# Optimization experiments

Measured on AMD Instinct MI355X. Metric: run time of the kernel, lower is better.

The kernel has to match this reference:

```python
import jax, jax.numpy as jnp
import numpy as np
import math

B, S, D_MODEL, NHEAD, DFF = 4, 1024, 1024, 16, 4096
D_K = D_MODEL // NHEAD
EPS = 1e-5
FACTOR = 5  # ProbAttention factor


def setup_inputs() -> dict:
    key = jax.random.key(0)
    ks = jax.random.split(key, 16)
    def w(k, shape):
        return 0.02 * jax.random.normal(k, shape, jnp.float32)
    inp = {
        "tgt": jax.random.normal(ks[0], (B, S, D_MODEL), jnp.float32),
        "memory": jax.random.normal(ks[1], (B, S, D_MODEL), jnp.float32),
    }
    i = 2
    for n in ["sa_wq", "sa_wk", "sa_wv", "sa_wo", "ca_wq", "ca_wk", "ca_wv", "ca_wo"]:
        inp[n] = w(ks[i], (D_MODEL, D_MODEL)); i += 1
        inp[n.replace("_w", "_b")] = jnp.zeros((D_MODEL,), jnp.float32)
    inp["w1"] = w(ks[i], (D_MODEL, DFF)); i += 1
    inp["b1"] = jnp.zeros((DFF,), jnp.float32)
    inp["w2"] = w(ks[i], (DFF, D_MODEL)); i += 1
    inp["b2"] = jnp.zeros((D_MODEL,), jnp.float32)
    for j in (1, 2, 3):
        inp[f"bn{j}_g"] = jnp.ones((D_MODEL,), jnp.float32)
        inp[f"bn{j}_b"] = jnp.zeros((D_MODEL,), jnp.float32)
    return inp


def prob_attention(q, k, v, rng):
    # Informer ProbSparse attention, mask_flag=False. q,k,v: [B,H,L,D]
    Bq, H, Lq, D = q.shape
    Lk = k.shape[2]
    sample_k = min(FACTOR * int(math.ceil(math.log(Lk))), Lk)
    n_top = min(FACTOR * int(math.ceil(math.log(Lq))), Lq)
    # sampled key indices per query position (shared across B,H, as in Informer)
    idx = jax.random.randint(rng, (Lq, sample_k), 0, Lk)
    k_samp = k[:, :, idx, :]                                 # [B,H,Lq,sample_k,D]
    qk_samp = jnp.einsum("bhld,bhlsd->bhls", q, k_samp)
    M = qk_samp.max(-1) - qk_samp.sum(-1) / Lk               # sparsity measure [B,H,Lq]
    top_idx = jax.lax.top_k(M, n_top)[1]                     # [B,H,n_top]
    q_red = jnp.take_along_axis(q, top_idx[..., None], axis=2)  # [B,H,n_top,D]
    scores = jnp.einsum("bhud,bhkd->bhuk", q_red, k) * (1.0 / math.sqrt(D))
    attn = jax.nn.softmax(scores, axis=-1)                   # [B,H,n_top,Lk]
    # initial context: mean of V for all queries, then overwrite the top queries
    ctx = jnp.broadcast_to(v.mean(axis=2, keepdims=True), (Bq, H, Lq, D))
    upd = jnp.einsum("bhuk,bhkd->bhud", attn, v)
    b_ix = jnp.arange(Bq)[:, None, None]
    h_ix = jnp.arange(H)[None, :, None]
    return ctx.at[b_ix, h_ix, top_idx].set(upd)


def mha(xq, xk, xv, wq, bq, wk, bk, wv, bv, wo, bo, rng):
    Bq, L, E = xq.shape
    def split(x, wt, bt):
        return (x @ wt + bt).reshape(Bq, L, NHEAD, D_K).transpose(0, 2, 1, 3)
    q, k, v = split(xq, wq, bq), split(xk, wk, bk), split(xv, wv, bv)
    o = prob_attention(q, k, v, rng)
    return o.transpose(0, 2, 1, 3).reshape(Bq, L, E) @ wo + bo


def bn(x, g, b):
    # BatchNorm1d over channel dim E, stats over (B, S) (training-mode, biased var)
    mu = x.mean(axis=(0, 1))
    var = x.var(axis=(0, 1))
    return (x - mu) * jax.lax.rsqrt(var + EPS) * g + b


def reference(tgt, memory, sa_wq, sa_bq, sa_wk, sa_bk, sa_wv, sa_bv, sa_wo, sa_bo,
              ca_wq, ca_bq, ca_wk, ca_bk, ca_wv, ca_bv, ca_wo, ca_bo,
              w1, b1, w2, b2, bn1_g, bn1_b, bn2_g, bn2_b, bn3_g, bn3_b):
    k1, k2 = jax.random.split(jax.random.key(42))
    t2 = mha(tgt, tgt, tgt, sa_wq, sa_bq, sa_wk, sa_bk, sa_wv, sa_bv, sa_wo, sa_bo, k1)
    x = bn(tgt + t2, bn1_g, bn1_b)
    t2 = mha(x, memory, memory, ca_wq, ca_bq, ca_wk, ca_bk, ca_wv, ca_bv, ca_wo, ca_bo, k2)
    x = bn(x + t2, bn2_g, bn2_b)
    t2 = jax.nn.gelu(x @ w1 + b1, approximate=False) @ w2 + b2
    return bn(x + t2, bn3_g, bn3_b)
```

## Files before the change

### kernel.cpp

```cpp
#include <hip/hip_runtime.h>
#include <cstdint>

#define BQ 4
#define SEQ 1024
#define EMB 1024
#define NH 16
#define DKH 64
#define DFF 4096
#define MROWS 4096
#define NSAMP 35
#define QKV_LD 3072

typedef int   i32x4 __attribute__((ext_vector_type(4)));
typedef float f32x4 __attribute__((ext_vector_type(4)));
typedef short s16x8 __attribute__((ext_vector_type(8)));
typedef __bf16 b16x8 __attribute__((ext_vector_type(8)));

__device__ __forceinline__ unsigned short bf16b(float f) {
  unsigned u = __builtin_bit_cast(unsigned, f);
  return (unsigned short)((u + 0x7FFFu + ((u >> 16) & 1u)) >> 16);
}

template <typename T> struct other_vec { using type = b16x8; };
template <> struct other_vec<b16x8>    { using type = s16x8; };

template <typename T>
__device__ __forceinline__ auto mfma_try(T a, T b, f32x4 c, int)
    -> decltype(__builtin_amdgcn_mfma_f32_16x16x32_bf16(a, b, c, 0, 0, 0)) {
  return __builtin_amdgcn_mfma_f32_16x16x32_bf16(a, b, c, 0, 0, 0);
}
template <typename T>
__device__ __forceinline__ f32x4 mfma_try(T a, T b, f32x4 c, long) {
  using U = typename other_vec<T>::type;
  U a2 = __builtin_bit_cast(U, a);
  U b2 = __builtin_bit_cast(U, b);
  return __builtin_amdgcn_mfma_f32_16x16x32_bf16(a2, b2, c, 0, 0, 0);
}
__device__ __forceinline__ f32x4 mfma_bf16(i32x4 a, i32x4 b, f32x4 c) {
  s16x8 as = __builtin_bit_cast(s16x8, a);
  s16x8 bs = __builtin_bit_cast(s16x8, b);
  return mfma_try(as, bs, c, 0);
}

typedef const __attribute__((address_space(1))) void GV;
typedef __attribute__((address_space(3))) void LV;
__device__ __forceinline__ void gload_lds16(const void* g, void* l) {
  __builtin_amdgcn_global_load_lds((GV*)(uintptr_t)g,
                                   (LV*)(unsigned)(uintptr_t)l, 16, 0, 0);
}

__device__ __forceinline__ void tf2x32(unsigned k0, unsigned k1, unsigned x0, unsigned x1,
                                       unsigned& o0, unsigned& o1) {
  unsigned ks2 = k0 ^ k1 ^ 0x1BD11BDAu;
  x0 += k0; x1 += k1;
#define TFR(r) { x0 += x1; x1 = (x1 << r) | (x1 >> (32 - r)); x1 ^= x0; }
  TFR(13) TFR(15) TFR(26) TFR(6)   x0 += k1;  x1 += ks2 + 1u;
  TFR(17) TFR(29) TFR(16) TFR(24)  x0 += ks2; x1 += k0 + 2u;
  TFR(13) TFR(15) TFR(26) TFR(6)   x0 += k0;  x1 += k1 + 3u;
  TFR(17) TFR(29) TFR(16) TFR(24)  x0 += k1;  x1 += ks2 + 4u;
  TFR(13) TFR(15) TFR(26) TFR(6)   x0 += ks2; x1 += k0 + 5u;
#undef TFR
  o0 = x0; o1 = x1;
}

__global__ void idx_kernel(int* __restrict__ out) {
  int t = blockIdx.x * 256 + threadIdx.x;
  if (t >= 2 * SEQ * NSAMP) return;
  int sel = t >= SEQ * NSAMP;
  int i = sel ? t - SEQ * NSAMP : t;
  unsigned s0, s1, d0, d1;
  tf2x32(0u, 42u, 0u, 0u, s0, s1);
  tf2x32(0u, 42u, 0u, 1u, d0, d1);
  unsigned key0 = sel ? d0 : s0, key1 = sel ? d1 : s1;
  unsigned o0, o1;
  tf2x32(key0, key1, 0u, (unsigned)i, o0, o1);
  out[t] = (int)((o0 ^ o1) & 1023u);
}

__global__ void f2b_kernel(const float* __restrict__ in, unsigned short* __restrict__ out, int n4) {
  int i = blockIdx.x * 256 + threadIdx.x;
  if (i >= n4) return;
  float4 v = ((const float4*)in)[i];
  uint2 p;
  p.x = (unsigned)bf16b(v.x) | ((unsigned)bf16b(v.y) << 16);
  p.y = (unsigned)bf16b(v.z) | ((unsigned)bf16b(v.w) << 16);
  ((uint2*)out)[i] = p;
}

__global__ void transpose_kernel(const float* __restrict__ W, unsigned short* __restrict__ WT,
                                 int K, int N) {
  __shared__ float tile[32][33];
  int n0 = blockIdx.x * 32, k0 = blockIdx.y * 32;
  int tx = threadIdx.x, ty = threadIdx.y;
#pragma unroll
  for (int r = 0; r < 4; ++r)
    tile[ty * 4 + r][tx] = W[(size_t)(k0 + ty * 4 + r) * N + n0 + tx];
  __syncthreads();
#pragma unroll
  for (int r = 0; r < 4; ++r) {
    int n = n0 + ty * 4 + r, k = k0 + tx;
    WT[(size_t)n * K + k] = bf16b(tile[tx][ty * 4 + r]);
  }
}

__global__ void biascat_kernel(const float* q, const float* k, const float* v,
                               const float* ck, const float* cv,
                               float* qkvB, float* kvB) {
  int t = blockIdx.x * 256 + threadIdx.x;
  if (t < 1024) {
    qkvB[t] = q[t]; qkvB[1024 + t] = k[t]; qkvB[2048 + t] = v[t];
    kvB[t] = ck[t]; kvB[1024 + t] = cv[t];
  }
}

template <int EPI>
__global__ __launch_bounds__(256) void gemm_kernel(
    const unsigned short* __restrict__ A, int lda,
    const unsigned short* __restrict__ BT, int ldb,
    float* __restrict__ C, int ldc,
    unsigned short* __restrict__ Cb, int ldcb,
    const float* __restrict__ bias, int K) {
  __shared__ alignas(16) unsigned short As[128 * 32];
  __shared__ alignas(16) unsigned short Bs[128 * 32];
  const int tid = threadIdx.x;
  const int bm = blockIdx.y << 7, bn = blockIdx.x << 7;
  const int wave = tid >> 6, lane = tid & 63;
  const int wm = (wave & 1) << 6, wn = (wave >> 1) << 6;
  const int lr = lane & 15, lg = lane >> 4;

  f32x4 acc[4][4];
#pragma unroll
  for (int i = 0; i < 4; ++i)
#pragma unroll
    for (int j = 0; j < 4; ++j) acc[i][j] = f32x4{0.f, 0.f, 0.f, 0.f};

  const int trow = tid >> 2, tcol = (tid & 3) << 3;
  const unsigned short* Ag = A + (size_t)(bm + trow) * lda + tcol;
  const unsigned short* Bg = BT + (size_t)(bn + trow) * ldb + tcol;
  unsigned short* Al = &As[tid * 8];
  unsigned short* Bl = &Bs[tid * 8];

  for (int kt = 0; kt < K; kt += 32) {
    __syncthreads();
    gload_lds16(Ag + kt, Al);
    gload_lds16(Ag + (size_t)64 * lda + kt, Al + 2048);
    gload_lds16(Bg + kt, Bl);
    gload_lds16(Bg + (size_t)64 * ldb + kt, Bl + 2048);
    __syncthreads();
    i32x4 af[4], bf[4];
#pragma unroll
    for (int i = 0; i < 4; ++i)
      af[i] = *(const i32x4*)&As[(wm + i * 16 + lr) * 32 + lg * 8];
#pragma unroll
    for (int j = 0; j < 4; ++j)
      bf[j] = *(const i32x4*)&Bs[(wn + j * 16 + lr) * 32 + lg * 8];
#pragma unroll
    for (int i = 0; i < 4; ++i)
#pragma unroll
      for (int j = 0; j < 4; ++j)
        acc[i][j] = mfma_bf16(af[i], bf[j], acc[i][j]);
  }
#pragma unroll
  for (int i = 0; i < 4; ++i)
#pragma unroll
    for (int j = 0; j < 4; ++j)
#pragma unroll
      for (int r = 0; r < 4; ++r) {
        int row = bm + wm + i * 16 + lg * 4 + r;
        int col = bn + wn + j * 16 + lr;
        float v = acc[i][j][r] + bias[col];
        if constexpr (EPI == 0) {
          C[(size_t)row * ldc + col] = v;
        } else {
          float gl = 0.5f * v * (1.f + erff(v * 0.70710678118654752f));
          Cb[(size_t)row * ldcb + col] = bf16b(gl);
        }
      }
}

__global__ __launch_bounds__(256) void m2_kernel(
    const float* __restrict__ QKV, const int* __restrict__ idx,
    float* __restrict__ Mout, int qcol, int kcol) {
  const int bh = blockIdx.y, qc = blockIdx.x;
  const int b = bh >> 4, h = bh & 15;
  const int tid = threadIdx.x, wv = tid >> 6, lane = tid & 63;
  const float* Qb = QKV + (size_t)b * SEQ * QKV_LD + qcol + h * 64;
  const float* Kb = QKV + (size_t)b * SEQ * QKV_LD + kcol + h * 64;
  const bool act = lane < NSAMP;
  for (int j = 0; j < 32; ++j) {
    int l = qc * 128 + wv * 32 + j;
    float dot = 0.f;
    if (act) {
      int sidx = idx[l * NSAMP + lane];
      const float* Kr = Kb + (size_t)sidx * QKV_LD;
      const float* Qr = Qb + (size_t)l * QKV_LD;
#pragma unroll
      for (int d4 = 0; d4 < 16; ++d4) {
        float4 k4 = *(const float4*)(Kr + d4 * 4);
        float4 q4 = *(const float4*)(Qr + d4 * 4);
        dot = fmaf(k4.x, q4.x, dot);
        dot = fmaf(k4.y, q4.y, dot);
        dot = fmaf(k4.z, q4.z, dot);
        dot = fmaf(k4.w, q4.w, dot);
      }
    }
    float mval = act ? dot : -__builtin_inff();
    float sval = act ? dot : 0.f;
#pragma unroll
    for (int m = 1; m < 64; m <<= 1) {
      mval = fmaxf(mval, __shfl_xor(mval, m, 64));
      sval += __shfl_xor(sval, m, 64);
    }
    if (lane == 0) Mout[bh * 1024 + l] = mval - sval * (1.f / 1024.f);
  }
}

__device__ __forceinline__ void amax2(float& v, int& id, float v2, int id2) {
  if (v2 > v || (v2 == v && id2 < id)) { v = v2; id = id2; }
}
__global__ __launch_bounds__(64) void topk2_kernel(
    const float* __restrict__ Mbuf, int* __restrict__ topOut) {
  const int bh = blockIdx.x, t = threadIdx.x;
  float v[16]; int li[16];
#pragma unroll
  for (int r = 0; r < 16; ++r) { int l = t + (r << 6); v[r] = Mbuf[bh * 1024 + l]; li[r] = l; }
  for (int it = 0; it < NSAMP; ++it) {
    float bv = v[0]; int bi = li[0];
#pragma unroll
    for (int r = 1; r < 16; ++r) amax2(bv, bi, v[r], li[r]);
#pragma unroll
    for (int m = 1; m < 64; m <<= 1) {
      float ov = __shfl_xor(bv, m, 64); int oi = __shfl_xor(bi, m, 64);
      amax2(bv, bi, ov, oi);
    }
    if (t == 0) topOut[bh * NSAMP + it] = bi;
#pragma unroll
    for (int r = 0; r < 16; ++r) if (li[r] == bi) v[r] = -__builtin_inff();
  }
}

__global__ void vmean_kernel(const float* __restrict__ QKV, float* __restrict__ vmean, int vcol) {
  const int g = blockIdx.x, bh = g >> 3, ch = g & 7;
  const int b = bh >> 4, h = bh & 15, d = threadIdx.x;
  const float* Vb = QKV + (size_t)b * SEQ * QKV_LD + vcol + h * 64 + d;
  float s = 0.f;
  for (int l = ch * 128; l < ch * 128 + 128; ++l) s += Vb[(size_t)l * QKV_LD];
  atomicAdd(&vmean[bh * 64 + d], s);
}

__global__ void fillO_kernel(const float* __restrict__ vmean, unsigned short* __restrict__ Ob) {
  int i = blockIdx.x * 256 + threadIdx.x;
  int e = i & 1023, b = i >> 20;
  int h = e >> 6, d = e & 63;
  Ob[i] = bf16b(vmean[((b << 4) + h) * 64 + d] * (1.f / 1024.f));
}

__global__ __launch_bounds__(256) void attn_part_kernel(
    const float* __restrict__ QKV, const int* __restrict__ topIdx,
    float* __restrict__ Opart, int qcol, int kcol, int vcol) {
  __shared__ int til[NSAMP];
  __shared__ alignas(16) float qs[NSAMP * 64];
  __shared__ alignas(16) float ps[NSAMP * 260];
  const int c = blockIdx.x, bh = blockIdx.y;
  const int b = bh >> 4, h = bh & 15;
  const int tid = threadIdx.x, wv = tid >> 6, lane = tid & 63;
  if (tid < NSAMP) til[tid] = topIdx[bh * NSAMP + tid];
  __syncthreads();
  for (int e = tid; e < NSAMP * 64; e += 256) {
    int i = e >> 6, d = e & 63;
    qs[e] = QKV[((size_t)b * SEQ + til[i]) * QKV_LD + qcol + h * 64 + d];
  }
  __syncthreads();
  {
    const float* Kr = QKV + ((size_t)b * SEQ + c * 256 + tid) * QKV_LD + kcol + h * 64;
    float acc[NSAMP];
#pragma unroll
    for (int i = 0; i < NSAMP; ++i) acc[i] = 0.f;
    for (int c16 = 0; c16 < 16; ++c16) {
      float4 k4 = *(const float4*)(Kr + c16 * 4);
#pragma unroll
      for (int i = 0; i < NSAMP; ++i) {
        float4 q4 = *(const float4*)&qs[i * 64 + c16 * 4];
        acc[i] = fmaf(k4.x, q4.x, acc[i]);
        acc[i] = fmaf(k4.y, q4.y, acc[i]);
        acc[i] = fmaf(k4.z, q4.z, acc[i]);
        acc[i] = fmaf(k4.w, q4.w, acc[i]);
      }
    }
#pragma unroll
    for (int i = 0; i < NSAMP; ++i) ps[i * 260 + tid] = expf(acc[i] * 0.125f);
  }
  __syncthreads();
  float o[NSAMP], sacc[NSAMP];
#pragma unroll
  for (int i = 0; i < NSAMP; ++i) { o[i] = 0.f; sacc[i] = 0.f; }
  {
    const float* Vb = QKV + ((size_t)b * SEQ + c * 256) * QKV_LD + vcol + h * 64 + lane;
    for (int j = 0; j < 64; ++j) {
      int kkl = wv * 64 + j;
      float vv = Vb[(size_t)kkl * QKV_LD];
#pragma unroll
      for (int i = 0; i < NSAMP; ++i) {
        float p = ps[i * 260 + kkl];
        o[i] = fmaf(p, vv, o[i]);
        sacc[i] += p;
      }
    }
  }
  __syncthreads();
  float* red = ps;
#pragma unroll
  for (int i = 0; i < NSAMP; ++i) {
    red[(wv * NSAMP + i) * 65 + lane] = o[i];
    if (lane == 0) red[(wv * NSAMP + i) * 65 + 64] = sacc[i];
  }
  __syncthreads();
  for (int e = tid; e < NSAMP * 65; e += 256) {
    int i = e / 65, d = e - i * 65;
    float s = red[(0 * NSAMP + i) * 65 + d] + red[(1 * NSAMP + i) * 65 + d] +
              red[(2 * NSAMP + i) * 65 + d] + red[(3 * NSAMP + i) * 65 + d];
    Opart[((size_t)(bh * NSAMP + i) * 4 + c) * 65 + d] = s;
  }
}

__global__ __launch_bounds__(256) void attn_final_kernel(
    const float* __restrict__ Opart, const int* __restrict__ topIdx,
    unsigned short* __restrict__ Ob) {
  int e = blockIdx.x * 256 + threadIdx.x;
  int d = e & 63, r = e >> 6;
  int bh = r / NSAMP, i = r - bh * NSAMP;
  const float* base = Opart + (size_t)r * 4 * 65;
  float s = base[d] + base[65 + d] + base[130 + d] + base[195 + d];
  float den = base[64] + base[129] + base[194] + base[259];
  int b = bh >> 4, h = bh & 15;
  int til = topIdx[r];
  Ob[((size_t)b * SEQ + til) * EMB + h * 64 + d] = bf16b(s / den);
}

__global__ __launch_bounds__(256) void bnstats_kernel(
    const float* __restrict__ a, const float* __restrict__ bb, float* __restrict__ sums) {
  const int t = threadIdx.x, r0 = blockIdx.x << 5;
  float s1[4] = {0, 0, 0, 0}, s2[4] = {0, 0, 0, 0};
  for (int r = r0; r < r0 + 32; ++r) {
    const float* ar = a + (size_t)r * EMB;
    const float* br = bb + (size_t)r * EMB;
#pragma unroll
    for (int q = 0; q < 4; ++q) {
      float x = ar[t + (q << 8)] + br[t + (q << 8)];
      s1[q] += x; s2[q] = fmaf(x, x, s2[q]);
    }
  }
#pragma unroll
  for (int q = 0; q < 4; ++q) {
    atomicAdd(&sums[t + (q << 8)], s1[q]);
    atomicAdd(&sums[EMB + t + (q << 8)], s2[q]);
  }
}
__global__ void bnapply_kernel(
    const float* __restrict__ a, const float* __restrict__ bres,
    const float* __restrict__ sums, const float* __restrict__ g,
    const float* __restrict__ bet, float* __restrict__ outF, unsigned short* __restrict__ outB) {
  int i = blockIdx.x * 256 + threadIdx.x;
  int c = i & (EMB - 1);
  float mu = sums[c] * (1.f / 4096.f);
  float var = sums[EMB + c] * (1.f / 4096.f) - mu * mu;
  float x = a[i] + bres[i];
  float y = (x - mu) * rsqrtf(var + 1e-5f) * g[c] + bet[c];
  outF[i] = y;
  if (outB) outB[i] = bf16b(y);
}

extern "C" void kernel_launch(void* const* d_in, const int* in_sizes, int n_in,
                              void* d_out, int out_size, void* d_ws, size_t ws_size,
                              hipStream_t stream) {
  const float* tgt  = (const float*)d_in[0];
  const float* memi = (const float*)d_in[1];
  const float* sa_wq = (const float*)d_in[2];  const float* sa_bq = (const float*)d_in[3];
  const float* sa_wk = (const float*)d_in[4];  const float* sa_bk = (const float*)d_in[5];
  const float* sa_wv = (const float*)d_in[6];  const float* sa_bv = (const float*)d_in[7];
  const float* sa_wo = (const float*)d_in[8];  const float* sa_bo = (const float*)d_in[9];
  const float* ca_wq = (const float*)d_in[10]; const float* ca_bq = (const float*)d_in[11];
  const float* ca_wk = (const float*)d_in[12]; const float* ca_bk = (const float*)d_in[13];
  const float* ca_wv = (const float*)d_in[14]; const float* ca_bv = (const float*)d_in[15];
  const float* ca_wo = (const float*)d_in[16]; const float* ca_bo = (const float*)d_in[17];
  const float* w1 = (const float*)d_in[18];    const float* b1 = (const float*)d_in[19];
  const float* w2 = (const float*)d_in[20];    const float* b2 = (const float*)d_in[21];
  const float* bn1g = (const float*)d_in[22];  const float* bn1b = (const float*)d_in[23];
  const float* bn2g = (const float*)d_in[24];  const float* bn2b = (const float*)d_in[25];
  const float* bn3g = (const float*)d_in[26];  const float* bn3b = (const float*)d_in[27];

  char* wsb = (char*)d_ws;
  size_t off = 0;
  auto alloc = [&](size_t bytes) -> char* {
    char* p = wsb + off;
    off = (off + bytes + 255) & ~(size_t)255;
    return p;
  };
  unsigned short* WTqkv = (unsigned short*)alloc((size_t)3072 * 1024 * 2);
  unsigned short* WTosa = (unsigned short*)alloc((size_t)1024 * 1024 * 2);
  unsigned short* WTqca = (unsigned short*)alloc((size_t)1024 * 1024 * 2);
  unsigned short* WTkv  = (unsigned short*)alloc((size_t)2048 * 1024 * 2);
  unsigned short* WToca = (unsigned short*)alloc((size_t)1024 * 1024 * 2);
  unsigned short* WT1   = (unsigned short*)alloc((size_t)4096 * 1024 * 2);
  unsigned short* WT2   = (unsigned short*)alloc((size_t)1024 * 4096 * 2);
  float* qkvB = (float*)alloc(3072 * 4);
  float* kvB  = (float*)alloc(2048 * 4);
  unsigned short* tgtB = (unsigned short*)alloc((size_t)MROWS * EMB * 2);
  unsigned short* memB = (unsigned short*)alloc((size_t)MROWS * EMB * 2);
  unsigned short* x1B  = (unsigned short*)alloc((size_t)MROWS * EMB * 2);
  unsigned short* x2B  = (unsigned short*)alloc((size_t)MROWS * EMB * 2);
  unsigned short* OB   = (unsigned short*)alloc((size_t)MROWS * EMB * 2);
  unsigned short* HB   = (unsigned short*)alloc((size_t)MROWS * DFF * 2);
  float* QKV = (float*)alloc((size_t)MROWS * QKV_LD * 4);
  float* t2  = (float*)alloc((size_t)MROWS * EMB * 4);
  float* x1f = (float*)alloc((size_t)MROWS * EMB * 4);
  float* x2f = (float*)alloc((size_t)MROWS * EMB * 4);
  int* idxb  = (int*)alloc((size_t)2 * SEQ * NSAMP * 4);
  float* Mbuf = (float*)alloc((size_t)64 * 1024 * 4);
  int* topA = (int*)alloc(64 * NSAMP * 4);
  int* topB = (int*)alloc(64 * NSAMP * 4);
  float* vmean = (float*)alloc(64 * 64 * 4);
  float* sums = (float*)alloc(2 * EMB * 4);
  float* Opart = (float*)alloc((size_t)64 * NSAMP * 4 * 65 * 4);
  if (off > ws_size) return;

  auto GEMM = [&](const unsigned short* A, int lda, const unsigned short* BT, int ldb,
                  float* C, int ldc, const float* bias, int M_, int N_, int K_) {
    dim3 g(N_ >> 7, M_ >> 7);
    gemm_kernel<0><<<g, 256, 0, stream>>>(A, lda, BT, ldb, C, ldc, nullptr, 0, bias, K_);
  };
  auto GEMMG = [&](const unsigned short* A, int lda, const unsigned short* BT, int ldb,
                   unsigned short* Cb, int ldcb, const float* bias, int M_, int N_, int K_) {
    dim3 g(N_ >> 7, M_ >> 7);
    gemm_kernel<1><<<g, 256, 0, stream>>>(A, lda, BT, ldb, nullptr, 0, Cb, ldcb, bias, K_);
  };
  auto TR = [&](const float* src, unsigned short* dst, int K_, int N_) {
    dim3 g(N_ / 32, K_ / 32), bl(32, 8);
    transpose_kernel<<<g, bl, 0, stream>>>(src, dst, K_, N_);
  };
  auto ATTN = [&](const float* qkv, const int* top) {
    (void)hipMemsetAsync(vmean, 0, 64 * 64 * 4, stream);
    vmean_kernel<<<512, 64, 0, stream>>>(qkv, vmean, 2048);
    fillO_kernel<<<16384, 256, 0, stream>>>(vmean, OB);
    attn_part_kernel<<<dim3(4, 64), 256, 0, stream>>>(qkv, top, Opart, 0, 1024, 2048);
    attn_final_kernel<<<560, 256, 0, stream>>>(Opart, top, OB);
  };

  idx_kernel<<<280, 256, 0, stream>>>(idxb);
  f2b_kernel<<<4096, 256, 0, stream>>>(tgt, tgtB, MROWS * EMB / 4);
  f2b_kernel<<<4096, 256, 0, stream>>>(memi, memB, MROWS * EMB / 4);
  TR(sa_wq, WTqkv, 1024, 1024);
  TR(sa_wk, WTqkv + (size_t)1024 * 1024, 1024, 1024);
  TR(sa_wv, WTqkv + (size_t)2048 * 1024, 1024, 1024);
  TR(sa_wo, WTosa, 1024, 1024);
  TR(ca_wq, WTqca, 1024, 1024);
  TR(ca_wk, WTkv, 1024, 1024);
  TR(ca_wv, WTkv + (size_t)1024 * 1024, 1024, 1024);
  TR(ca_wo, WToca, 1024, 1024);
  TR(w1, WT1, 1024, 4096);
  TR(w2, WT2, 4096, 1024);
  biascat_kernel<<<4, 256, 0, stream>>>(sa_bq, sa_bk, sa_bv, ca_bk, ca_bv, qkvB, kvB);

  GEMM(tgtB, 1024, WTqkv, 1024, QKV, QKV_LD, qkvB, MROWS, 3072, 1024);
  m2_kernel<<<dim3(8, 64), 256, 0, stream>>>(QKV, idxb, Mbuf, 0, 1024);
  topk2_kernel<<<64, 64, 0, stream>>>(Mbuf, topA);
  ATTN(QKV, topA);
  GEMM(OB, 1024, WTosa, 1024, t2, 1024, sa_bo, MROWS, 1024, 1024);
  (void)hipMemsetAsync(sums, 0, 2 * EMB * 4, stream);
  bnstats_kernel<<<128, 256, 0, stream>>>(tgt, t2, sums);
  bnapply_kernel<<<16384, 256, 0, stream>>>(tgt, t2, sums, bn1g, bn1b, x1f, x1B);

  GEMM(x1B, 1024, WTqca, 1024, QKV, QKV_LD, ca_bq, MROWS, 1024, 1024);
  GEMM(memB, 1024, WTkv, 1024, QKV + 1024, QKV_LD, kvB, MROWS, 2048, 1024);
  m2_kernel<<<dim3(8, 64), 256, 0, stream>>>(QKV, idxb + SEQ * NSAMP, Mbuf, 0, 1024);
  topk2_kernel<<<64, 64, 0, stream>>>(Mbuf, topB);
  ATTN(QKV, topB);
  GEMM(OB, 1024, WToca, 1024, t2, 1024, ca_bo, MROWS, 1024, 1024);
  (void)hipMemsetAsync(sums, 0, 2 * EMB * 4, stream);
  bnstats_kernel<<<128, 256, 0, stream>>>(x1f, t2, sums);
  bnapply_kernel<<<16384, 256, 0, stream>>>(x1f, t2, sums, bn2g, bn2b, x2f, x2B);

  GEMMG(x2B, 1024, WT1, 1024, HB, DFF, b1, MROWS, DFF, 1024);
  GEMM(HB, 4096, WT2, 4096, t2, 1024, b2, MROWS, 1024, 4096);
  (void)hipMemsetAsync(sums, 0, 2 * EMB * 4, stream);
  bnstats_kernel<<<128, 256, 0, stream>>>(x2f, t2, sums);
  bnapply_kernel<<<16384, 256, 0, stream>>>(x2f, t2, sums, bn3g, bn3b, (float*)d_out, nullptr);
}
```

Measured before the change: 1.048 ms.

## Write QKV projections in head-major layout and remap attention blocks per XCD

The QKV projection GEMMs now scatter their output into a head-major [which][b*h][l][d] layout instead of a row-major 3072-wide matrix. The sparsity-measure, V-mean and attention kernels then read contiguous 256-byte rows per head rather than striding by 3072 floats. Block indices are also remapped so blocks working on the same heads land on the same XCD, aiming for better L2 reuse. The GEMM epilogue writes become more scattered, which could cost some store efficiency.

```diff
diff --git a/kernel.cpp b/kernel.cpp
--- a/kernel.cpp
+++ b/kernel.cpp
@@ -119,7 +119,7 @@
     const unsigned short* __restrict__ BT, int ldb,
     float* __restrict__ C, int ldc,
     unsigned short* __restrict__ Cb, int ldcb,
-    const float* __restrict__ bias, int K) {
+    const float* __restrict__ bias, int K, int colofs) {
   __shared__ alignas(16) unsigned short As[128 * 32];
   __shared__ alignas(16) unsigned short Bs[128 * 32];
   const int tid = threadIdx.x;
@@ -171,29 +171,37 @@
         float v = acc[i][j][r] + bias[col];
         if constexpr (EPI == 0) {
           C[(size_t)row * ldc + col] = v;
-        } else {
+        } else if constexpr (EPI == 1) {
           float gl = 0.5f * v * (1.f + erff(v * 0.70710678118654752f));
           Cb[(size_t)row * ldcb + col] = bf16b(gl);
+        } else {
+          int cc = col + colofs;
+          int which = cc >> 10;
+          int h = (cc >> 6) & 15;
+          int d = col & 63;
+          int b = row >> 10, l = row & 1023;
+          C[((size_t)which << 22) + (((b << 4) + h) << 16) + (l << 6) + d] = v;
         }
       }
 }
 
-__global__ __launch_bounds__(256) void m2_kernel(
-    const float* __restrict__ QKV, const int* __restrict__ idx,
-    float* __restrict__ Mout, int qcol, int kcol) {
-  const int bh = blockIdx.y, qc = blockIdx.x;
-  const int b = bh >> 4, h = bh & 15;
+__global__ __launch_bounds__(256) void m3_kernel(
+    const float* __restrict__ Qh, const float* __restrict__ Kh,
+    const int* __restrict__ idx, float* __restrict__ Mout) {
+  const int id = blockIdx.x;
+  const int xcd = id & 7, slot = id >> 3;
+  const int bh = xcd * 8 + (slot & 7), qc = slot >> 3;
   const int tid = threadIdx.x, wv = tid >> 6, lane = tid & 63;
-  const float* Qb = QKV + (size_t)b * SEQ * QKV_LD + qcol + h * 64;
-  const float* Kb = QKV + (size_t)b * SEQ * QKV_LD + kcol + h * 64;
+  const float* Qb = Qh + ((size_t)bh << 16);
+  const float* Kb = Kh + ((size_t)bh << 16);
   const bool act = lane < NSAMP;
   for (int j = 0; j < 32; ++j) {
     int l = qc * 128 + wv * 32 + j;
     float dot = 0.f;
     if (act) {
       int sidx = idx[l * NSAMP + lane];
-      const float* Kr = Kb + (size_t)sidx * QKV_LD;
-      const float* Qr = Qb + (size_t)l * QKV_LD;
+      const float* Kr = Kb + ((size_t)sidx << 6);
+      const float* Qr = Qb + ((size_t)l << 6);
 #pragma unroll
       for (int d4 = 0; d4 < 16; ++d4) {
         float4 k4 = *(const float4*)(Kr + d4 * 4);
@@ -239,12 +247,12 @@
   }
 }
 
-__global__ void vmean_kernel(const float* __restrict__ QKV, float* __restrict__ vmean, int vcol) {
+__global__ void vmean_kernel(const float* __restrict__ Vh, float* __restrict__ vmean) {
   const int g = blockIdx.x, bh = g >> 3, ch = g & 7;
-  const int b = bh >> 4, h = bh & 15, d = threadIdx.x;
-  const float* Vb = QKV + (size_t)b * SEQ * QKV_LD + vcol + h * 64 + d;
+  const int d = threadIdx.x;
+  const float* Vb = Vh + ((size_t)bh << 16) + (ch * 128 << 6) + d;
   float s = 0.f;
-  for (int l = ch * 128; l < ch * 128 + 128; ++l) s += Vb[(size_t)l * QKV_LD];
+  for (int l = 0; l < 128; ++l) s += Vb[l << 6];
   atomicAdd(&vmean[bh * 64 + d], s);
 }
 
@@ -256,23 +264,24 @@
 }
 
 __global__ __launch_bounds__(256) void attn_part_kernel(
-    const float* __restrict__ QKV, const int* __restrict__ topIdx,
-    float* __restrict__ Opart, int qcol, int kcol, int vcol) {
+    const float* __restrict__ Qh, const float* __restrict__ Kh, const float* __restrict__ Vh,
+    const int* __restrict__ topIdx, float* __restrict__ Opart) {
   __shared__ int til[NSAMP];
   __shared__ alignas(16) float qs[NSAMP * 64];
   __shared__ alignas(16) float ps[NSAMP * 260];
-  const int c = blockIdx.x, bh = blockIdx.y;
-  const int b = bh >> 4, h = bh & 15;
+  const int id = blockIdx.x;
+  const int xcd = id & 7, slot = id >> 3;
+  const int bh = xcd * 8 + (slot & 7), c = slot >> 3;
   const int tid = threadIdx.x, wv = tid >> 6, lane = tid & 63;
   if (tid < NSAMP) til[tid] = topIdx[bh * NSAMP + tid];
   __syncthreads();
   for (int e = tid; e < NSAMP * 64; e += 256) {
     int i = e >> 6, d = e & 63;
-    qs[e] = QKV[((size_t)b * SEQ + til[i]) * QKV_LD + qcol + h * 64 + d];
+    qs[e] = Qh[((size_t)bh << 16) + ((size_t)til[i] << 6) + d];
   }
   __syncthreads();
   {
-    const float* Kr = QKV + ((size_t)b * SEQ + c * 256 + tid) * QKV_LD + kcol + h * 64;
+    const float* Kr = Kh + ((size_t)bh << 16) + ((size_t)(c * 256 + tid) << 6);
     float acc[NSAMP];
 #pragma unroll
     for (int i = 0; i < NSAMP; ++i) acc[i] = 0.f;
@@ -295,10 +304,10 @@
 #pragma unroll
   for (int i = 0; i < NSAMP; ++i) { o[i] = 0.f; sacc[i] = 0.f; }
   {
-    const float* Vb = QKV + ((size_t)b * SEQ + c * 256) * QKV_LD + vcol + h * 64 + lane;
+    const float* Vb = Vh + ((size_t)bh << 16) + ((size_t)(c * 256) << 6) + lane;
     for (int j = 0; j < 64; ++j) {
       int kkl = wv * 64 + j;
-      float vv = Vb[(size_t)kkl * QKV_LD];
+      float vv = Vb[(size_t)kkl << 6];
 #pragma unroll
       for (int i = 0; i < NSAMP; ++i) {
         float p = ps[i * 260 + kkl];
@@ -411,7 +420,7 @@
   unsigned short* x2B  = (unsigned short*)alloc((size_t)MROWS * EMB * 2);
   unsigned short* OB   = (unsigned short*)alloc((size_t)MROWS * EMB * 2);
   unsigned short* HB   = (unsigned short*)alloc((size_t)MROWS * DFF * 2);
-  float* QKV = (float*)alloc((size_t)MROWS * QKV_LD * 4);
+  float* QKVh = (float*)alloc((size_t)3 * 64 * 65536 * 4);
   float* t2  = (float*)alloc((size_t)MROWS * EMB * 4);
   float* x1f = (float*)alloc((size_t)MROWS * EMB * 4);
   float* x2f = (float*)alloc((size_t)MROWS * EMB * 4);
@@ -424,25 +433,34 @@
   float* Opart = (float*)alloc((size_t)64 * NSAMP * 4 * 65 * 4);
   if (off > ws_size) return;
 
+  float* Qh = QKVh;
+  float* Kh = QKVh + ((size_t)1 << 22);
+  float* Vh = QKVh + ((size_t)2 << 22);
+
   auto GEMM = [&](const unsigned short* A, int lda, const unsigned short* BT, int ldb,
                   float* C, int ldc, const float* bias, int M_, int N_, int K_) {
     dim3 g(N_ >> 7, M_ >> 7);
-    gemm_kernel<0><<<g, 256, 0, stream>>>(A, lda, BT, ldb, C, ldc, nullptr, 0, bias, K_);
+    gemm_kernel<0><<<g, 256, 0, stream>>>(A, lda, BT, ldb, C, ldc, nullptr, 0, bias, K_, 0);
   };
   auto GEMMG = [&](const unsigned short* A, int lda, const unsigned short* BT, int ldb,
                    unsigned short* Cb, int ldcb, const float* bias, int M_, int N_, int K_) {
     dim3 g(N_ >> 7, M_ >> 7);
-    gemm_kernel<1><<<g, 256, 0, stream>>>(A, lda, BT, ldb, nullptr, 0, Cb, ldcb, bias, K_);
+    gemm_kernel<1><<<g, 256, 0, stream>>>(A, lda, BT, ldb, nullptr, 0, Cb, ldcb, bias, K_, 0);
+  };
+  auto GEMMH = [&](const unsigned short* A, const unsigned short* BT,
+                   const float* bias, int N_, int K_, int colofs) {
+    dim3 g(N_ >> 7, MROWS >> 7);
+    gemm_kernel<2><<<g, 256, 0, stream>>>(A, K_, BT, K_, QKVh, 0, nullptr, 0, bias, K_, colofs);
   };
   auto TR = [&](const float* src, unsigned short* dst, int K_, int N_) {
     dim3 g(N_ / 32, K_ / 32), bl(32, 8);
     transpose_kernel<<<g, bl, 0, stream>>>(src, dst, K_, N_);
   };
-  auto ATTN = [&](const float* qkv, const int* top) {
+  auto ATTN = [&](const int* top) {
     (void)hipMemsetAsync(vmean, 0, 64 * 64 * 4, stream);
-    vmean_kernel<<<512, 64, 0, stream>>>(qkv, vmean, 2048);
+    vmean_kernel<<<512, 64, 0, stream>>>(Vh, vmean);
     fillO_kernel<<<16384, 256, 0, stream>>>(vmean, OB);
-    attn_part_kernel<<<dim3(4, 64), 256, 0, stream>>>(qkv, top, Opart, 0, 1024, 2048);
+    attn_part_kernel<<<256, 256, 0, stream>>>(Qh, Kh, Vh, top, Opart);
     attn_final_kernel<<<560, 256, 0, stream>>>(Opart, top, OB);
   };
 
@@ -461,20 +479,20 @@
   TR(w2, WT2, 4096, 1024);
   biascat_kernel<<<4, 256, 0, stream>>>(sa_bq, sa_bk, sa_bv, ca_bk, ca_bv, qkvB, kvB);
 
-  GEMM(tgtB, 1024, WTqkv, 1024, QKV, QKV_LD, qkvB, MROWS, 3072, 1024);
-  m2_kernel<<<dim3(8, 64), 256, 0, stream>>>(QKV, idxb, Mbuf, 0, 1024);
+  GEMMH(tgtB, WTqkv, qkvB, 3072, 1024, 0);
+  m3_kernel<<<512, 256, 0, stream>>>(Qh, Kh, idxb, Mbuf);
   topk2_kernel<<<64, 64, 0, stream>>>(Mbuf, topA);
-  ATTN(QKV, topA);
+  ATTN(topA);
   GEMM(OB, 1024, WTosa, 1024, t2, 1024, sa_bo, MROWS, 1024, 1024);
   (void)hipMemsetAsync(sums, 0, 2 * EMB * 4, stream);
   bnstats_kernel<<<128, 256, 0, stream>>>(tgt, t2, sums);
   bnapply_kernel<<<16384, 256, 0, stream>>>(tgt, t2, sums, bn1g, bn1b, x1f, x1B);
 
-  GEMM(x1B, 1024, WTqca, 1024, QKV, QKV_LD, ca_bq, MROWS, 1024, 1024);
-  GEMM(memB, 1024, WTkv, 1024, QKV + 1024, QKV_LD, kvB, MROWS, 2048, 1024);
-  m2_kernel<<<dim3(8, 64), 256, 0, stream>>>(QKV, idxb + SEQ * NSAMP, Mbuf, 0, 1024);
+  GEMMH(x1B, WTqca, ca_bq, 1024, 1024, 0);
+  GEMMH(memB, WTkv, kvB, 2048, 1024, 1024);
+  m3_kernel<<<512, 256, 0, stream>>>(Qh, Kh, idxb + SEQ * NSAMP, Mbuf);
   topk2_kernel<<<64, 64, 0, stream>>>(Mbuf, topB);
-  ATTN(QKV, topB);
+  ATTN(topB);
   GEMM(OB, 1024, WToca, 1024, t2, 1024, ca_bo, MROWS, 1024, 1024);
   (void)hipMemsetAsync(sums, 0, 2 * EMB * 4, stream);
   bnstats_kernel<<<128, 256, 0, stream>>>(x1f, t2, sums);
```

Result: faster. 984.0 us (-6.1%).
